# Kernel optimization log

Measured on AMD Instinct MI355X. Metric: run time of the kernel, lower is better.

## Reference

```python
import jax, jax.numpy as jnp
import numpy as np

DIM = 1536
HEADS = 12
HD = DIM // HEADS           # 128
C = HD // 2                 # 64 rotary pairs per head
B = 1
F_, H_, W_ = 16, 16, 16
S = F_ * H_ * W_            # 4096
MAXPOS = 1024
EPS = 1e-6
SPLITS = (C - 2 * (C // 3), C // 3, C // 3)  # (22, 21, 21)


def setup_inputs() -> dict:
    key = jax.random.key(0)
    ks = jax.random.split(key, 8)
    std = 0.02
    x = jax.random.normal(ks[0], (B, S, DIM), jnp.float32)
    seq_lens = jnp.full((B,), S, dtype=jnp.int32)
    grid_sizes = jnp.tile(jnp.array([[F_, H_, W_]], jnp.int32), (B, 1))
    # rotary angle table: per split, theta_j = pos / 10000^(j/size)
    angs = []
    pos = jnp.arange(MAXPOS, dtype=jnp.float32)
    for sz in SPLITS:
        inv = 1.0 / (10000.0 ** (jnp.arange(sz, dtype=jnp.float32) / sz))
        angs.append(jnp.outer(pos, inv))
    freqs = jnp.concatenate(angs, axis=1)  # [MAXPOS, C]
    return {
        "x": x,
        "seq_lens": seq_lens,
        "grid_sizes": grid_sizes,
        "freqs": freqs,
        "wq": jax.random.normal(ks[1], (DIM, DIM), jnp.float32) * std,
        "bq": jnp.zeros((DIM,), jnp.float32),
        "wk": jax.random.normal(ks[2], (DIM, DIM), jnp.float32) * std,
        "bk": jnp.zeros((DIM,), jnp.float32),
        "wv": jax.random.normal(ks[3], (DIM, DIM), jnp.float32) * std,
        "bv": jnp.zeros((DIM,), jnp.float32),
        "wo": jax.random.normal(ks[4], (DIM, DIM), jnp.float32) * std,
        "bo": jnp.zeros((DIM,), jnp.float32),
        "gq": jnp.ones((DIM,), jnp.float32),
        "gk": jnp.ones((DIM,), jnp.float32),
    }


def _rms_norm(x, g):
    # x * rsqrt(mean(x^2) + eps) * g  (WanRMSNorm)
    var = jnp.mean(jnp.square(x), axis=-1, keepdims=True)
    return x * jax.lax.rsqrt(var + EPS) * g


def _rope(x, freqs, f, h, w):
    # x: [b, s, n, hd]; freqs: [MAXPOS, C] angles; grid (f,h,w), s = f*h*w
    fa = freqs[:f, : SPLITS[0]]
    ha = freqs[:h, SPLITS[0] : SPLITS[0] + SPLITS[1]]
    wa = freqs[:w, SPLITS[0] + SPLITS[1] :]
    ang = jnp.concatenate(
        [
            jnp.broadcast_to(fa[:, None, None, :], (f, h, w, SPLITS[0])),
            jnp.broadcast_to(ha[None, :, None, :], (f, h, w, SPLITS[1])),
            jnp.broadcast_to(wa[None, None, :, :], (f, h, w, SPLITS[2])),
        ],
        axis=-1,
    ).reshape(f * h * w, 1, C)  # [s, 1, C] broadcasts over heads
    cos, sin = jnp.cos(ang), jnp.sin(ang)
    xr = x[..., 0::2]  # real parts of complex pairs
    xi = x[..., 1::2]  # imag parts
    out_r = xr * cos - xi * sin
    out_i = xr * sin + xi * cos
    return jnp.stack([out_r, out_i], axis=-1).reshape(x.shape)


def reference(x, seq_lens, grid_sizes, freqs, wq, bq, wk, bk, wv, bv, wo, bo, gq, gk):
    b, s = x.shape[:2]
    q = _rms_norm(x @ wq.T + bq, gq).reshape(b, s, HEADS, HD)
    k = _rms_norm(x @ wk.T + bk, gk).reshape(b, s, HEADS, HD)
    v = (x @ wv.T + bv).reshape(b, s, HEADS, HD)
    # all samples share the same grid (static for jit)
    q = _rope(q, freqs, F_, H_, W_)
    k = _rope(k, freqs, F_, H_, W_)
    scale = 1.0 / np.sqrt(HD)
    scores = jnp.einsum("bqnd,bknd->bnqk", q, k) * scale  # [b, n, s, s]
    k_pos = jnp.arange(s)
    mask = k_pos[None, None, None, :] < seq_lens[:, None, None, None]
    scores = scores + jnp.where(mask, 0.0, -1e9)
    attn = jax.nn.softmax(scores, axis=-1)
    out = jnp.einsum("bnqk,bknd->bqnd", attn, v).reshape(b, s, DIM)
    return out @ wo.T + bo
```

## Files before the change

kernel.cpp:

```cpp
#include <hip/hip_runtime.h>
#include <hip/hip_bf16.h>

#define DIM   1536
#define HEADS 12
#define HD    128
#define SEQ   4096
#define QSCALE 0.08838834764831845f
#define LOG2E 1.44269504088896f

typedef __attribute__((ext_vector_type(8))) short short8;
typedef __attribute__((ext_vector_type(4))) float f32x4;
typedef __attribute__((ext_vector_type(16))) float f32x16;

__device__ __forceinline__ unsigned short f2bf(float f) {
    __hip_bfloat16 h = __float2bfloat16(f);
    return *reinterpret_cast<unsigned short*>(&h);
}
__device__ __forceinline__ float bf2f(unsigned short u) {
    return __uint_as_float(((unsigned int)u) << 16);
}
__device__ __forceinline__ void async_cp16(void* lds, const void* g) {
    __builtin_amdgcn_global_load_lds(
        (const __attribute__((address_space(1))) unsigned int*)g,
        (__attribute__((address_space(3))) unsigned int*)lds, 16, 0, 0);
}

__global__ __launch_bounds__(256) void convert_bf16(
    const float* __restrict__ src, __hip_bfloat16* __restrict__ dst, int n8)
{
    const int i = blockIdx.x * 256 + threadIdx.x;
    if (i >= n8) return;
    const float4 a = *reinterpret_cast<const float4*>(src + (size_t)i * 8);
    const float4 b = *reinterpret_cast<const float4*>(src + (size_t)i * 8 + 4);
    uint4 o;
    o.x = (unsigned int)f2bf(a.x) | ((unsigned int)f2bf(a.y) << 16);
    o.y = (unsigned int)f2bf(a.z) | ((unsigned int)f2bf(a.w) << 16);
    o.z = (unsigned int)f2bf(b.x) | ((unsigned int)f2bf(b.y) << 16);
    o.w = (unsigned int)f2bf(b.z) | ((unsigned int)f2bf(b.w) << 16);
    *reinterpret_cast<uint4*>(dst + (size_t)i * 8) = o;
}

__global__ __launch_bounds__(256) void convert_all(
    const float* __restrict__ x,  const float* __restrict__ wq,
    const float* __restrict__ wk, const float* __restrict__ wv,
    __hip_bfloat16* __restrict__ xb,  __hip_bfloat16* __restrict__ wqb,
    __hip_bfloat16* __restrict__ wkb, __hip_bfloat16* __restrict__ wvb)
{
    const int i = blockIdx.x * 256 + threadIdx.x;
    const float* src;
    __hip_bfloat16* dst;
    int off;
    if (i < 786432)            { src = x;  dst = xb;  off = i; }
    else if (i < 1081344)      { src = wq; dst = wqb; off = i - 786432; }
    else if (i < 1376256)      { src = wk; dst = wkb; off = i - 1081344; }
    else                       { src = wv; dst = wvb; off = i - 1376256; }
    const float4 a = *reinterpret_cast<const float4*>(src + (size_t)off * 8);
    const float4 b = *reinterpret_cast<const float4*>(src + (size_t)off * 8 + 4);
    uint4 o;
    o.x = (unsigned int)f2bf(a.x) | ((unsigned int)f2bf(a.y) << 16);
    o.y = (unsigned int)f2bf(a.z) | ((unsigned int)f2bf(a.w) << 16);
    o.z = (unsigned int)f2bf(b.x) | ((unsigned int)f2bf(b.y) << 16);
    o.w = (unsigned int)f2bf(b.z) | ((unsigned int)f2bf(b.w) << 16);
    *reinterpret_cast<uint4*>(dst + (size_t)off * 8) = o;
}

__global__ __launch_bounds__(256) void gemm_qkv(
    const __hip_bfloat16* __restrict__ xb,
    const __hip_bfloat16* __restrict__ wqb, const float* __restrict__ bq,
    const __hip_bfloat16* __restrict__ wkb, const float* __restrict__ bk,
    const __hip_bfloat16* __restrict__ wvb, const float* __restrict__ bv,
    __hip_bfloat16* __restrict__ yq, __hip_bfloat16* __restrict__ yk,
    __hip_bfloat16* __restrict__ vrow)
{
    __shared__ __align__(16) short As[128][32];
    __shared__ __align__(16) short Bs[128][32];
    const int z  = blockIdx.z;
    const __hip_bfloat16* W = (z == 0) ? wqb : (z == 1) ? wkb : wvb;
    const float* bias = (z == 0) ? bq : (z == 1) ? bk : bv;
    __hip_bfloat16* outp = (z == 0) ? yq : (z == 1) ? yk : vrow;
    const int bm0 = blockIdx.x * 128;
    const int bn0 = blockIdx.y * 128;
    const int tid  = threadIdx.x;
    const int lane = tid & 63;
    const int wid  = tid >> 6;
    const int wm = (wid >> 1) * 64;
    const int wn = (wid & 1)  * 64;
    const int fr = lane & 15;
    const int fc = (lane >> 4) * 8;
    const int srow = tid >> 2;
    const int scol = (tid & 3) * 8;

    f32x4 acc[4][4] = {};

    for (int kt = 0; kt < DIM; kt += 32) {
        #pragma unroll
        for (int i = 0; i < 2; i++) {
            async_cp16(&As[i * 64 + ((tid >> 6) << 4)][0],
                       xb + (size_t)(bm0 + i * 64 + srow) * DIM + kt + scol);
            async_cp16(&Bs[i * 64 + ((tid >> 6) << 4)][0],
                       W + (size_t)(bn0 + i * 64 + srow) * DIM + kt + scol);
        }
        __syncthreads();
        short8 af[4], bf8[4];
        #pragma unroll
        for (int m = 0; m < 4; m++) af[m]  = *reinterpret_cast<const short8*>(&As[wm + m * 16 + fr][fc]);
        #pragma unroll
        for (int n = 0; n < 4; n++) bf8[n] = *reinterpret_cast<const short8*>(&Bs[wn + n * 16 + fr][fc]);
        #pragma unroll
        for (int m = 0; m < 4; m++)
            #pragma unroll
            for (int n = 0; n < 4; n++)
                acc[m][n] = __builtin_amdgcn_mfma_f32_16x16x32_bf16(af[m], bf8[n], acc[m][n], 0, 0, 0);
        __syncthreads();
    }

    const int crow0 = bm0 + wm + (lane >> 4) * 4;
    const int ccol0 = bn0 + wn + fr;
    #pragma unroll
    for (int n = 0; n < 4; n++) {
        const int col = ccol0 + n * 16;
        const float bb = bias[col];
        #pragma unroll
        for (int m = 0; m < 4; m++)
            #pragma unroll
            for (int r = 0; r < 4; r++)
                outp[(size_t)(crow0 + m * 16 + r) * DIM + col] =
                    __float2bfloat16(acc[m][n][r] + bb);
    }
}

__global__ __launch_bounds__(256) void norm_rope_transpose(
    __hip_bfloat16* __restrict__ yq, __hip_bfloat16* __restrict__ yk,
    const float* __restrict__ gq, const float* __restrict__ gk,
    const float* __restrict__ freqs,
    const __hip_bfloat16* __restrict__ vrow, __hip_bfloat16* __restrict__ vT)
{
    __shared__ float red[4];
    __shared__ __align__(16) short tile[64][72];
    const int b = blockIdx.x;
    const int t = threadIdx.x;

    if (b < 8192) {
        const int s = b >> 1;
        const int z = b & 1;
        __hip_bfloat16* y = z ? yk : yq;
        const float* g = z ? gk : gq;

        float xr[3], xi[3];
        float ss = 0.f;
        #pragma unroll
        for (int i = 0; i < 3; i++) {
            const int p = t + i * 256;
            const unsigned int uu = *reinterpret_cast<const unsigned int*>(&y[(size_t)s * DIM + 2 * p]);
            xr[i] = bf2f((unsigned short)(uu & 0xffffu));
            xi[i] = bf2f((unsigned short)(uu >> 16));
            ss += xr[i] * xr[i] + xi[i] * xi[i];
        }
        #pragma unroll
        for (int m = 1; m < 64; m <<= 1) ss += __shfl_xor(ss, m, 64);
        if ((t & 63) == 0) red[t >> 6] = ss;
        __syncthreads();
        const float sum = red[0] + red[1] + red[2] + red[3];
        const float rs = rsqrtf(sum * (1.0f / DIM) + 1e-6f);
        const int f = s >> 8, hh = (s >> 4) & 15, ww = s & 15;
        const float osc = z ? 1.0f : QSCALE;
        #pragma unroll
        for (int i = 0; i < 3; i++) {
            const int p = t + i * 256;
            const int cc = p & 63;
            const int pos = (cc < 22) ? f : (cc < 43) ? hh : ww;
            const float ang = freqs[pos * 64 + cc];
            float sn, cs;
            sincosf(ang, &sn, &cs);
            const float a = xr[i] * rs * g[2 * p];
            const float bb = xi[i] * rs * g[2 * p + 1];
            const unsigned int pk = (unsigned int)f2bf((a * cs - bb * sn) * osc)
                                  | ((unsigned int)f2bf((a * sn + bb * cs) * osc) << 16);
            *reinterpret_cast<unsigned int*>(&y[(size_t)s * DIM + 2 * p]) = pk;
        }
    } else {
        const int tb = b - 8192;
        const int s0 = (tb & 63) * 64;
        const int c0 = (tb >> 6) * 64;
        #pragma unroll
        for (int i = 0; i < 2; i++) {
            const int ch = t + i * 256;
            const int r = ch >> 3, cc = (ch & 7) * 8;
            *reinterpret_cast<int4*>(&tile[r][cc]) =
                *reinterpret_cast<const int4*>(&vrow[(size_t)(s0 + r) * DIM + c0 + cc]);
        }
        __syncthreads();
        #pragma unroll
        for (int i = 0; i < 2; i++) {
            const int ch = t + i * 256;
            const int c = ch & 63, sc = (ch >> 6) * 8;
            unsigned int w0 = (unsigned short)tile[sc + 0][c] | ((unsigned int)(unsigned short)tile[sc + 1][c] << 16);
            unsigned int w1 = (unsigned short)tile[sc + 2][c] | ((unsigned int)(unsigned short)tile[sc + 3][c] << 16);
            unsigned int w2 = (unsigned short)tile[sc + 4][c] | ((unsigned int)(unsigned short)tile[sc + 5][c] << 16);
            unsigned int w3 = (unsigned short)tile[sc + 6][c] | ((unsigned int)(unsigned short)tile[sc + 7][c] << 16);
            int4 val;
            val.x = (int)w0; val.y = (int)w1; val.z = (int)w2; val.w = (int)w3;
            *reinterpret_cast<int4*>(&vT[(size_t)(c0 + c) * SEQ + s0 + sc]) = val;
        }
    }
}

__global__ __launch_bounds__(256, 2) void flash_attn(
    const __hip_bfloat16* __restrict__ qb,
    const __hip_bfloat16* __restrict__ kb,
    const __hip_bfloat16* __restrict__ vT,
    const int* __restrict__ seq_lens,
    __hip_bfloat16* __restrict__ attno)
{
    __shared__ __align__(16) short Ks[2][64][128];
    __shared__ __align__(16) short Vs[3][128][64];
    const int qt = blockIdx.x;
    const int h  = blockIdx.y;
    const int tid = threadIdx.x;
    const int lane = tid & 63;
    const int w = tid >> 6;
    const int q5 = lane & 31;
    const int hi = lane >> 5;
    const int seqlen = seq_lens[0];
    const int swz = (lane & 7) << 4;
    const int NT = SEQ / 64;

    short8 qf[8];
    const int qrow = qt * 128 + w * 32 + q5;
    #pragma unroll
    for (int s = 0; s < 8; s++)
        qf[s] = *reinterpret_cast<const short8*>(&qb[(size_t)qrow * DIM + h * HD + s * 16 + hi * 8]);

    f32x16 oacc[4] = {};
    float m = -1e30f, l = 0.f;
    unsigned int WpG[4][4];

    const int kROW = w * 4 + (lane >> 4);
    const int kCOL = ((lane & 15) ^ (kROW & 7)) * 8;
    const int vROW = w * 8 + (lane >> 3);
    const int vCOL = (((lane & 7) ^ (vROW & 7))) * 8;

    auto stageK = [&](int tile, int slot) {
        #pragma unroll
        for (int i = 0; i < 4; i++)
            async_cp16(&Ks[slot][i * 16 + w * 4][0],
                       kb + (size_t)(tile * 64 + i * 16 + kROW) * DIM + h * HD + kCOL);
    };
    auto stageV = [&](int tile, int slot) {
        #pragma unroll
        for (int i = 0; i < 4; i++)
            async_cp16(&Vs[slot][i * 32 + vROW][0],
                       vT + ((size_t)h * HD + i * 32 + vROW) * SEQ + tile * 64 + vCOL);
    };
    auto pv = [&](int slot) {
        const char* Vp = (const char*)&Vs[slot][0][0];
        __builtin_amdgcn_s_setprio(1);
        #pragma unroll
        for (int ks = 0; ks < 4; ks++) {
            int4 pwv;
            pwv.x = (int)WpG[ks][0];
            pwv.y = (int)WpG[ks][1];
            pwv.z = (int)WpG[ks][2];
            pwv.w = (int)WpG[ks][3];
            const short8 pf = __builtin_bit_cast(short8, pwv);
            #pragma unroll
            for (int cb = 0; cb < 4; cb++) {
                short8 vf = *reinterpret_cast<const short8*>(
                    Vp + (cb * 32 + q5) * 128 + ((ks * 32 + hi * 16) ^ swz));
                oacc[cb] = __builtin_amdgcn_mfma_f32_32x32x16_bf16(vf, pf, oacc[cb], 0, 0, 0);
            }
        }
        __builtin_amdgcn_s_setprio(0);
    };
    auto softmax_pack = [&](int tt, f32x16* S) {
        const int kbase = tt * 64;
        float v[32];
        if (kbase + 64 <= seqlen) {
            #pragma unroll
            for (int kbk = 0; kbk < 2; kbk++)
                #pragma unroll
                for (int r = 0; r < 16; r++) v[kbk * 16 + r] = S[kbk][r];
        } else {
            #pragma unroll
            for (int kbk = 0; kbk < 2; kbk++)
                #pragma unroll
                for (int r = 0; r < 16; r++) {
                    const int key = kbase + kbk * 32 + (r & 3) + 8 * (r >> 2) + 4 * hi;
                    const float sv = (key < seqlen) ? S[kbk][r] : -1e30f;
                    S[kbk][r] = sv;
                    v[kbk * 16 + r] = sv;
                }
        }
        #pragma unroll
        for (int st = 16; st >= 1; st >>= 1)
            #pragma unroll
            for (int i = 0; i < st; i++) v[i] = fmaxf(v[i], v[i + st]);
        float tmax = fmaxf(v[0], __shfl_xor(v[0], 32, 64));

        if (!__all(tmax <= m + 8.0f)) {
            const float mn = fmaxf(m, tmax);
            const float alpha = exp2f((m - mn) * LOG2E);
            m = mn;
            l *= alpha;
            #pragma unroll
            for (int cb = 0; cb < 4; cb++)
                #pragma unroll
                for (int r = 0; r < 16; r++) oacc[cb][r] *= alpha;
        }
        const float nmL = -m * LOG2E;
        #pragma unroll
        for (int kbk = 0; kbk < 2; kbk++)
            #pragma unroll
            for (int r = 0; r < 16; r++) {
                const float p = exp2f(fmaf(S[kbk][r], LOG2E, nmL));
                S[kbk][r] = p;
                v[kbk * 16 + r] = p;
            }
        #pragma unroll
        for (int st = 16; st >= 1; st >>= 1)
            #pragma unroll
            for (int i = 0; i < st; i++) v[i] += v[i + st];
        l += v[0] + __shfl_xor(v[0], 32, 64);

        unsigned int Wl[2][4][2];
        #pragma unroll
        for (int kbk = 0; kbk < 2; kbk++)
            #pragma unroll
            for (int tq = 0; tq < 4; tq++) {
                Wl[kbk][tq][0] = (unsigned int)f2bf(S[kbk][4 * tq + 0])
                               | ((unsigned int)f2bf(S[kbk][4 * tq + 1]) << 16);
                Wl[kbk][tq][1] = (unsigned int)f2bf(S[kbk][4 * tq + 2])
                               | ((unsigned int)f2bf(S[kbk][4 * tq + 3]) << 16);
            }
        #pragma unroll
        for (int ks = 0; ks < 4; ks++) {
            const int kbk = ks >> 1;
            const int te = (ks & 1) * 2, to = te + 1;
            const int a0 = (int)Wl[kbk][te][0], a1 = (int)Wl[kbk][te][1];
            const int b0 = (int)Wl[kbk][to][0], b1 = (int)Wl[kbk][to][1];
            const int xa0 = __shfl_xor(a0, 32, 64);
            const int xa1 = __shfl_xor(a1, 32, 64);
            const int xb0 = __shfl_xor(b0, 32, 64);
            const int xb1 = __shfl_xor(b1, 32, 64);
            WpG[ks][0] = (unsigned int)(hi ? xb0 : a0);
            WpG[ks][1] = (unsigned int)(hi ? xb1 : a1);
            WpG[ks][2] = (unsigned int)(hi ? b0  : xa0);
            WpG[ks][3] = (unsigned int)(hi ? b1  : xa1);
        }
    };
    auto qk = [&](int slot, f32x16* S) {
        const char* Kp = (const char*)&Ks[slot][0][0];
        __builtin_amdgcn_s_setprio(1);
        #pragma unroll
        for (int s = 0; s < 8; s++)
            #pragma unroll
            for (int kbk = 0; kbk < 2; kbk++) {
                short8 kf = *reinterpret_cast<const short8*>(
                    Kp + (kbk * 32 + q5) * 256 + ((s * 32 + hi * 16) ^ swz));
                S[kbk] = __builtin_amdgcn_mfma_f32_32x32x16_bf16(kf, qf[s], S[kbk], 0, 0, 0);
            }
        __builtin_amdgcn_s_setprio(0);
    };

    stageK(0, 0); stageV(0, 0);
    __syncthreads();
    stageK(1, 1); stageV(1, 1);
    {
        f32x16 sacc[2] = {};
        qk(0, sacc);
        softmax_pack(0, sacc);
    }

    int vprev = 0, vnext = 2;
    for (int t = 1; t < NT; t++) {
        __syncthreads();
        if (t + 1 < NT) {
            stageK(t + 1, (t + 1) & 1);
            stageV(t + 1, vnext);
        }
        f32x16 sacc[2] = {};
        qk(t & 1, sacc);
        pv(vprev);
        softmax_pack(t, sacc);
        vprev = (vprev == 2) ? 0 : vprev + 1;
        vnext = (vnext == 2) ? 0 : vnext + 1;
    }

    pv(vprev);

    const float inv_l = 1.f / l;
    const size_t obase = (size_t)qrow * DIM + h * HD;
    #pragma unroll
    for (int cb = 0; cb < 4; cb++) {
        #pragma unroll
        for (int tq = 0; tq < 4; tq++) {
            uint2 pko;
            pko.x = (unsigned int)f2bf(oacc[cb][4 * tq + 0] * inv_l)
                  | ((unsigned int)f2bf(oacc[cb][4 * tq + 1] * inv_l) << 16);
            pko.y = (unsigned int)f2bf(oacc[cb][4 * tq + 2] * inv_l)
                  | ((unsigned int)f2bf(oacc[cb][4 * tq + 3] * inv_l) << 16);
            *reinterpret_cast<uint2*>(&attno[obase + cb * 32 + 8 * tq + 4 * hi]) = pko;
        }
    }
}

__global__ __launch_bounds__(256) void gemm_out(
    const __hip_bfloat16* __restrict__ A,
    const __hip_bfloat16* __restrict__ W,
    const float* __restrict__ bias,
    float* __restrict__ outp)
{
    __shared__ __align__(16) short As[128][32];
    __shared__ __align__(16) short Bs[128][32];
    const int bm0 = blockIdx.x * 128;
    const int bn0 = blockIdx.y * 128;
    const int tid = threadIdx.x;
    const int lane = tid & 63;
    const int wid = tid >> 6;
    const int wm = (wid >> 1) * 64;
    const int wn = (wid & 1) * 64;
    const int fr = lane & 15;
    const int fc = (lane >> 4) * 8;
    const int srow = tid >> 2;
    const int scol = (tid & 3) * 8;

    f32x4 acc[4][4] = {};

    for (int kt = 0; kt < DIM; kt += 32) {
        #pragma unroll
        for (int i = 0; i < 2; i++) {
            async_cp16(&As[i * 64 + ((tid >> 6) << 4)][0],
                       A + (size_t)(bm0 + i * 64 + srow) * DIM + kt + scol);
            async_cp16(&Bs[i * 64 + ((tid >> 6) << 4)][0],
                       W + (size_t)(bn0 + i * 64 + srow) * DIM + kt + scol);
        }
        __syncthreads();
        short8 af[4], bf8[4];
        #pragma unroll
        for (int m = 0; m < 4; m++) af[m]  = *reinterpret_cast<const short8*>(&As[wm + m * 16 + fr][fc]);
        #pragma unroll
        for (int n = 0; n < 4; n++) bf8[n] = *reinterpret_cast<const short8*>(&Bs[wn + n * 16 + fr][fc]);
        #pragma unroll
        for (int m = 0; m < 4; m++)
            #pragma unroll
            for (int n = 0; n < 4; n++)
                acc[m][n] = __builtin_amdgcn_mfma_f32_16x16x32_bf16(af[m], bf8[n], acc[m][n], 0, 0, 0);
        __syncthreads();
    }

    const int crow0 = bm0 + wm + (lane >> 4) * 4;
    const int ccol0 = bn0 + wn + fr;
    #pragma unroll
    for (int n = 0; n < 4; n++) {
        const int col = ccol0 + n * 16;
        const float bb = bias[col];
        #pragma unroll
        for (int m = 0; m < 4; m++)
            #pragma unroll
            for (int r = 0; r < 4; r++)
                outp[(size_t)(crow0 + m * 16 + r) * DIM + col] = acc[m][n][r] + bb;
    }
}

extern "C" void kernel_launch(void* const* d_in, const int* in_sizes, int n_in,
                              void* d_out, int out_size, void* d_ws, size_t ws_size,
                              hipStream_t stream)
{
    const float* x        = (const float*)d_in[0];
    const int*   seq_lens = (const int*)d_in[1];
    const float* freqs    = (const float*)d_in[3];
    const float* wq = (const float*)d_in[4];
    const float* bq = (const float*)d_in[5];
    const float* wk = (const float*)d_in[6];
    const float* bk = (const float*)d_in[7];
    const float* wv = (const float*)d_in[8];
    const float* bv = (const float*)d_in[9];
    const float* wo = (const float*)d_in[10];
    const float* bo = (const float*)d_in[11];
    const float* gq = (const float*)d_in[12];
    const float* gk = (const float*)d_in[13];
    float* out = (float*)d_out;

    char* ws = (char*)d_ws;
    __hip_bfloat16* yq    = (__hip_bfloat16*)(ws);
    __hip_bfloat16* yk    = (__hip_bfloat16*)(ws + 12582912);
    __hip_bfloat16* vrow  = (__hip_bfloat16*)(ws + 25165824);
    __hip_bfloat16* vT    = (__hip_bfloat16*)(ws + 37748736);
    __hip_bfloat16* attno = (__hip_bfloat16*)(ws + 25165824);
    __hip_bfloat16* xb    = (__hip_bfloat16*)(ws + 37748736);
    __hip_bfloat16* wob   = (__hip_bfloat16*)(ws);
    __hip_bfloat16* wqb   = (__hip_bfloat16*)d_out;
    __hip_bfloat16* wkb   = wqb + 2359296;
    __hip_bfloat16* wvb   = wkb + 2359296;

    dim3 blk(256);
    convert_all        <<<dim3(6528), blk, 0, stream>>>(x, wq, wk, wv, xb, wqb, wkb, wvb);
    gemm_qkv           <<<dim3(32, 12, 3), blk, 0, stream>>>(xb, wqb, bq, wkb, bk, wvb, bv, yq, yk, vrow);
    norm_rope_transpose<<<dim3(9728), blk, 0, stream>>>(yq, yk, gq, gk, freqs, vrow, vT);
    flash_attn         <<<dim3(32, 12), blk, 0, stream>>>(yq, yk, vT, seq_lens, attno);
    convert_bf16       <<<dim3(1152), blk, 0, stream>>>(wo, wob, 294912);
    gemm_out           <<<dim3(32, 12), blk, 0, stream>>>(attno, wob, bo, out);
}
```

Before: 324.0 us.

## Double-buffer LDS tiles and remap block order in QKV and output GEMMs

```diff
diff --git a/kernel.cpp b/kernel.cpp
--- a/kernel.cpp
+++ b/kernel.cpp
@@ -72,14 +72,20 @@
     __hip_bfloat16* __restrict__ yq, __hip_bfloat16* __restrict__ yk,
     __hip_bfloat16* __restrict__ vrow)
 {
-    __shared__ __align__(16) short As[128][32];
-    __shared__ __align__(16) short Bs[128][32];
-    const int z  = blockIdx.z;
+    __shared__ __align__(16) short As[2][128][32];
+    __shared__ __align__(16) short Bs[2][128][32];
+    const int bid = (blockIdx.z * 12 + blockIdx.y) * 32 + blockIdx.x;
+    const int tix = (bid & 7) * 144 + (bid >> 3);
+    const int z   = tix / 384;
+    const int rem = tix - z * 384;
+    const int by  = rem >> 5;
+    const int bx  = rem & 31;
+
     const __hip_bfloat16* W = (z == 0) ? wqb : (z == 1) ? wkb : wvb;
     const float* bias = (z == 0) ? bq : (z == 1) ? bk : bv;
     __hip_bfloat16* outp = (z == 0) ? yq : (z == 1) ? yk : vrow;
-    const int bm0 = blockIdx.x * 128;
-    const int bn0 = blockIdx.y * 128;
+    const int bm0 = bx * 128;
+    const int bn0 = by * 128;
     const int tid  = threadIdx.x;
     const int lane = tid & 63;
     const int wid  = tid >> 6;
@@ -92,20 +98,28 @@
 
     f32x4 acc[4][4] = {};
 
-    for (int kt = 0; kt < DIM; kt += 32) {
+    auto stage = [&](int kt, int buf) {
         #pragma unroll
         for (int i = 0; i < 2; i++) {
-            async_cp16(&As[i * 64 + ((tid >> 6) << 4)][0],
+            async_cp16(&As[buf][i * 64 + (wid << 4)][0],
                        xb + (size_t)(bm0 + i * 64 + srow) * DIM + kt + scol);
-            async_cp16(&Bs[i * 64 + ((tid >> 6) << 4)][0],
+            async_cp16(&Bs[buf][i * 64 + (wid << 4)][0],
                        W + (size_t)(bn0 + i * 64 + srow) * DIM + kt + scol);
         }
-        __syncthreads();
+    };
+
+    stage(0, 0);
+    __syncthreads();
+
+    const int NK = DIM / 32;
+    for (int k = 0; k < NK; k++) {
+        const int cur = k & 1;
+        if (k + 1 < NK) stage((k + 1) * 32, cur ^ 1);
         short8 af[4], bf8[4];
         #pragma unroll
-        for (int m = 0; m < 4; m++) af[m]  = *reinterpret_cast<const short8*>(&As[wm + m * 16 + fr][fc]);
-        #pragma unroll
-        for (int n = 0; n < 4; n++) bf8[n] = *reinterpret_cast<const short8*>(&Bs[wn + n * 16 + fr][fc]);
+        for (int m = 0; m < 4; m++) af[m]  = *reinterpret_cast<const short8*>(&As[cur][wm + m * 16 + fr][fc]);
+        #pragma unroll
+        for (int n = 0; n < 4; n++) bf8[n] = *reinterpret_cast<const short8*>(&Bs[cur][wn + n * 16 + fr][fc]);
         #pragma unroll
         for (int m = 0; m < 4; m++)
             #pragma unroll
@@ -410,10 +424,14 @@
     const float* __restrict__ bias,
     float* __restrict__ outp)
 {
-    __shared__ __align__(16) short As[128][32];
-    __shared__ __align__(16) short Bs[128][32];
-    const int bm0 = blockIdx.x * 128;
-    const int bn0 = blockIdx.y * 128;
+    __shared__ __align__(16) short As[2][128][32];
+    __shared__ __align__(16) short Bs[2][128][32];
+    const int bid = blockIdx.y * 32 + blockIdx.x;
+    const int tix = (bid & 7) * 48 + (bid >> 3);
+    const int by  = tix >> 5;
+    const int bx  = tix & 31;
+    const int bm0 = bx * 128;
+    const int bn0 = by * 128;
     const int tid = threadIdx.x;
     const int lane = tid & 63;
     const int wid = tid >> 6;
@@ -426,20 +444,28 @@
 
     f32x4 acc[4][4] = {};
 
-    for (int kt = 0; kt < DIM; kt += 32) {
+    auto stage = [&](int kt, int buf) {
         #pragma unroll
         for (int i = 0; i < 2; i++) {
-            async_cp16(&As[i * 64 + ((tid >> 6) << 4)][0],
+            async_cp16(&As[buf][i * 64 + (wid << 4)][0],
                        A + (size_t)(bm0 + i * 64 + srow) * DIM + kt + scol);
-            async_cp16(&Bs[i * 64 + ((tid >> 6) << 4)][0],
+            async_cp16(&Bs[buf][i * 64 + (wid << 4)][0],
                        W + (size_t)(bn0 + i * 64 + srow) * DIM + kt + scol);
         }
-        __syncthreads();
+    };
+
+    stage(0, 0);
+    __syncthreads();
+
+    const int NK = DIM / 32;
+    for (int k = 0; k < NK; k++) {
+        const int cur = k & 1;
+        if (k + 1 < NK) stage((k + 1) * 32, cur ^ 1);
         short8 af[4], bf8[4];
         #pragma unroll
-        for (int m = 0; m < 4; m++) af[m]  = *reinterpret_cast<const short8*>(&As[wm + m * 16 + fr][fc]);
-        #pragma unroll
-        for (int n = 0; n < 4; n++) bf8[n] = *reinterpret_cast<const short8*>(&Bs[wn + n * 16 + fr][fc]);
+        for (int m = 0; m < 4; m++) af[m]  = *reinterpret_cast<const short8*>(&As[cur][wm + m * 16 + fr][fc]);
+        #pragma unroll
+        for (int n = 0; n < 4; n++) bf8[n] = *reinterpret_cast<const short8*>(&Bs[cur][wn + n * 16 + fr][fc]);
         #pragma unroll
         for (int m = 0; m < 4; m++)
             #pragma unroll
```

After: 344.5 us. 6.3% more time.
